# Kernel tuning notes

Measured on AMD Instinct MI355X. Metric: run time of the kernel, lower is better.

## Reference

```python
import jax, jax.numpy as jnp
import numpy as np
import math

# neuralef_loss_cfg constants
T = 10.0
K_FEAT = 32          # num_nearestn_feature
K_PIX = ((10, 2.0), (10, 0.1))  # (num_nearestn_pixel{1,2}, distance_weight)
PIX_W = 0.05         # pixelwise_weight
ALPHA = 1.0


def setup_inputs() -> dict:
    key = jax.random.key(0)
    k1, k2, k3 = jax.random.split(key, 3)
    highlevel_feature = jax.random.normal(k1, (8, 1024, 768), dtype=jnp.float32)
    Psi = jax.random.normal(k2, (8, 1024, 64), dtype=jnp.float32)
    im = jax.random.normal(k3, (8, 3, 32, 32), dtype=jnp.float32)
    return {"highlevel_feature": highlevel_feature, "Psi": Psi, "im": im}


def _build_gram(highlevel_feature, im):
    """Feature kNN graph + pixel kNN graphs -> degree-normalized gram matrix."""
    bs, n, d = highlevel_feature.shape
    M = bs * n
    # --- feature affinity: cosine sim, mutual-ish kNN sparsification ---
    X = highlevel_feature.reshape(M, d)
    X = X / jnp.linalg.norm(X, axis=-1, keepdims=True)
    A = X @ X.T                                   # [M, M]
    A = A.at[jnp.diag_indices(M)].set(-jnp.inf)
    A = jnp.maximum(A, 0.0)                       # clamp(min=0); diag -inf -> 0
    vals, idx = jax.lax.top_k(A, K_FEAT)          # [M, K]
    res = jnp.zeros_like(A).at[jnp.arange(M)[:, None], idx].set(vals)
    A = (res + res.T) * 0.5

    # --- pixel affinity: RGB + weighted xy coordinates, euclidean kNN ---
    im = (im + 1.0) / 2.0
    h, w = im.shape[2], im.shape[3]
    hw = h * w
    x_ = jnp.tile(jnp.linspace(0.0, 1.0, w), (h,))          # [hw]
    y_ = jnp.repeat(jnp.linspace(0.0, 1.0, h), w)           # [hw]
    imf = im.reshape(bs, 3, hw).transpose(0, 2, 1)          # [bs, hw, 3]
    row = jnp.arange(hw)
    A_p = jnp.zeros((bs, hw, hw), dtype=bool)
    for k, dw in K_PIX:
        if k == 0:
            continue
        coords = jnp.broadcast_to(jnp.stack([x_ * dw, y_ * dw], -1), (bs, hw, 2))
        im2 = jnp.concatenate([imf, coords], axis=-1)       # [bs, hw, 5]
        sq = jnp.sum(im2 * im2, axis=-1)                    # [bs, hw]
        d2 = sq[:, :, None] + sq[:, None, :] - 2.0 * jnp.einsum('bnd,bmd->bnm', im2, im2)
        euc = -jnp.sqrt(jnp.maximum(d2, 0.0))               # -cdist
        euc = euc.at[:, row, row].set(-jnp.inf)
        _, pidx = jax.lax.top_k(euc, k)                     # [bs, hw, k]
        r = jnp.zeros((bs, hw, hw), dtype=bool).at[
            jnp.arange(bs)[:, None, None], row[None, :, None], pidx].set(True)
        A_p = A_p | r | r.transpose(0, 2, 1)

    A2 = jax.scipy.linalg.block_diag(*[A_p[i].astype(jnp.float32) for i in range(bs)])

    D = jax.lax.rsqrt(A.sum(-1))
    gram = A * D[None, :] * D[:, None]
    D2 = jax.lax.rsqrt(A2.sum(-1))
    gram2 = A2 * D2[None, :] * D2[:, None]
    return gram + gram2 * PIX_W                             # [M, M]


def reference(highlevel_feature, Psi, im):
    Psi = Psi.reshape(-1, Psi.shape[-1]) * math.sqrt(T)     # [M, kdim]
    gram = _build_gram(highlevel_feature, im)
    gP = gram @ Psi                                         # [M, kdim]
    R = Psi.T @ gP
    R_hat = jax.lax.stop_gradient(Psi).T @ gP               # no_sg = False
    kdim = Psi.shape[1]
    loss = -jnp.trace(R) / kdim
    reg = jnp.sum(jnp.triu(R_hat ** 2, 1)) / kdim
    return (loss, reg * ALPHA)
```

## Files before the change

kernel.cpp:

```cpp
#include <hip/hip_runtime.h>
#include <hip/hip_bf16.h>
#include <math.h>

constexpr int MT  = 8192;
constexpr int DF  = 768;
constexpr int KD  = 64;
constexpr int HWP = 1024;
constexpr int KF  = 32;
constexpr int KP  = 10;
constexpr int RPB = 512;
constexpr int CANDQ = 512;
constexpr int NTILE = 2080;
#define SQT 3.16227766016837933f
#define PIXW 0.05f
#define THR_BITS 0x2C7Bu

typedef __bf16 bf16x8 __attribute__((ext_vector_type(8)));
typedef __bf16 bf16x4 __attribute__((ext_vector_type(4)));
typedef float  f32x4  __attribute__((ext_vector_type(4)));
typedef unsigned u32x4 __attribute__((ext_vector_type(4)));
typedef unsigned short u16x8 __attribute__((ext_vector_type(8)));
typedef _Float16 f16;

__device__ inline void tile_map(int bid, int& ti, int& tj) {
  const int xcd = bid & 7;
  const int s = bid >> 3;
  const int p = s / 65, r = s % 65;
  const int c1 = xcd * 4 + p;
  if (r <= c1) { ti = r; tj = c1; }
  else         { ti = r - c1 - 1; tj = 63 - c1; }
}

__global__ __launch_bounds__(256) void prep_input_kernel(const float* __restrict__ X,
                                                         __bf16* __restrict__ Xb,
                                                         const float* __restrict__ im,
                                                         unsigned* __restrict__ pmask,
                                                         float* __restrict__ frow) {
  __shared__ float fr[HWP], fg[HWP], fb[HWP];
  __shared__ float red[256];
  const int tid = threadIdx.x;
  if (blockIdx.x < MT) {
    const int row = blockIdx.x;
    if (tid == 0) frow[row] = 0.f;
    const float4* xr4 = (const float4*)(X + (size_t)row * DF);
    float4 v = make_float4(0.f, 0.f, 0.f, 0.f);
    float s = 0.f;
    if (tid < 192) {
      v = xr4[tid];
      s = v.x * v.x + v.y * v.y + v.z * v.z + v.w * v.w;
    }
    red[tid] = s; __syncthreads();
    for (int o = 128; o > 0; o >>= 1) { if (tid < o) red[tid] += red[tid + o]; __syncthreads(); }
    const float rn = rsqrtf(red[0]);
    if (tid < 192) {
      bf16x4 o;
      o[0] = (__bf16)(v.x * rn); o[1] = (__bf16)(v.y * rn);
      o[2] = (__bf16)(v.z * rn); o[3] = (__bf16)(v.w * rn);
      *(bf16x4*)(Xb + (size_t)row * DF + tid * 4) = o;
    }
    return;
  }
  const int bx = blockIdx.x - MT;
  const int lane = tid & 63, wv = tid >> 6;
  const int b = bx >> 8;
  const int p = ((bx & 255) << 2) + wv;
  const float* imb = im + (size_t)b * 3 * HWP;
  for (int q = tid; q < HWP; q += 256) {
    fr[q] = imb[q]; fg[q] = imb[HWP + q]; fb[q] = imb[2 * HWP + q];
  }
  __syncthreads();
  const float pr = fr[p], pg = fg[p], pb = fb[p];
  const float px = (float)(p & 31) * (1.f / 31.f), py = (float)(p >> 5) * (1.f / 31.f);
  float d0[16], d1[16];
  #pragma unroll
  for (int i = 0; i < 16; ++i) {
    const int q = lane + (i << 6);
    float dr = (fr[q] - pr) * 0.5f, dg = (fg[q] - pg) * 0.5f, db = (fb[q] - pb) * 0.5f;
    float drgb = dr * dr + dg * dg + db * db;
    float dx = (float)(q & 31) * (1.f / 31.f) - px;
    float dy = (float)(q >> 5) * (1.f / 31.f) - py;
    float cd = dx * dx + dy * dy;
    d0[i] = (q == p) ? 1e30f : drgb + 4.00f * cd;
    d1[i] = (q == p) ? 1e30f : drgb + 0.01f * cd;
  }
  const int mrow = (b << 10) + p;
  auto doPass = [&](float (&dd)[16]) {
    for (int it = 0; it < KP; ++it) {
      float bm = 1e30f; int bq = 0;
      #pragma unroll
      for (int i = 0; i < 16; ++i) {
        const int q = lane + (i << 6);
        if (dd[i] < bm) { bm = dd[i]; bq = q; }
      }
      #pragma unroll
      for (int o = 32; o > 0; o >>= 1) {
        float ov = __shfl_down(bm, o);
        int   oq = __shfl_down(bq, o);
        if (ov < bm) { bm = ov; bq = oq; }
      }
      bq = __shfl(bq, 0);
      if (lane == 0) {
        atomicOr(&pmask[(size_t)mrow * 32 + (bq >> 5)], 1u << (bq & 31));
        atomicOr(&pmask[((size_t)((b << 10) + bq)) * 32 + (p >> 5)], 1u << (p & 31));
      }
      #pragma unroll
      for (int i = 0; i < 16; ++i)
        if (lane + (i << 6) == bq) dd[i] = 1e30f;
    }
  };
  doPass(d0);
  doPass(d1);
}

union SMem {
  struct { __bf16 A[128 * 64]; __bf16 B[128 * 64]; } st;
  f16 T[128 * 128];
};

__global__ __launch_bounds__(256) void gemm_kernel(const __bf16* __restrict__ Xb,
                                                   f16* __restrict__ S) {
  __shared__ SMem sm;
  const int tid = threadIdx.x;
  const int lane = tid & 63;
  const int wv = tid >> 6;
  const int wm = (wv & 1) * 64, wn = (wv >> 1) * 64;
  const int l15 = lane & 15, lq = lane >> 4;
  const int lr8 = lane >> 3, lc8 = lane & 7;
  const int rsw = l15 & 7;

  int ti, tj;
  tile_map(blockIdx.x, ti, tj);
  const int m0 = ti * 128;
  const int n0 = tj * 128;

  f32x4 acc[4][4];
  #pragma unroll
  for (int i = 0; i < 4; ++i)
    #pragma unroll
    for (int j = 0; j < 4; ++j)
      #pragma unroll
      for (int q = 0; q < 4; ++q) acc[i][j][q] = 0.f;

  for (int kt = 0; kt < 12; ++kt) {
    const int col0 = kt * 64;
    const __bf16* Ag = Xb + (size_t)m0 * DF + col0;
    const __bf16* Bg = Xb + (size_t)n0 * DF + col0;
    #pragma unroll
    for (int i = 0; i < 4; ++i) {
      const int r0 = (wv * 4 + i) * 8;
      const int csw = (lc8 ^ lr8) * 8;
      __builtin_amdgcn_global_load_lds(
          (const __attribute__((address_space(1))) void*)(Ag + (size_t)(r0 + lr8) * DF + csw),
          (__attribute__((address_space(3))) void*)(&sm.st.A[r0 * 64]), 16, 0, 0);
      __builtin_amdgcn_global_load_lds(
          (const __attribute__((address_space(1))) void*)(Bg + (size_t)(r0 + lr8) * DF + csw),
          (__attribute__((address_space(3))) void*)(&sm.st.B[r0 * 64]), 16, 0, 0);
    }
    __syncthreads();
    #pragma unroll
    for (int kk = 0; kk < 64; kk += 32) {
      bf16x8 af[4], bg[4];
      #pragma unroll
      for (int i = 0; i < 4; ++i)
        af[i] = *(const bf16x8*)(&sm.st.A[(wm + i * 16 + l15) * 64 + ((((kk >> 3) + lq) ^ rsw) * 8)]);
      #pragma unroll
      for (int j = 0; j < 4; ++j)
        bg[j] = *(const bf16x8*)(&sm.st.B[(wn + j * 16 + l15) * 64 + ((((kk >> 3) + lq) ^ rsw) * 8)]);
      #pragma unroll
      for (int i = 0; i < 4; ++i)
        #pragma unroll
        for (int j = 0; j < 4; ++j)
          acc[i][j] = __builtin_amdgcn_mfma_f32_16x16x32_bf16(af[i], bg[j], acc[i][j], 0, 0, 0);
    }
    __syncthreads();
  }
  #pragma unroll
  for (int i = 0; i < 4; ++i)
    #pragma unroll
    for (int j = 0; j < 4; ++j)
      #pragma unroll
      for (int q = 0; q < 4; ++q) {
        const int tr = wm + i * 16 + lq * 4 + q;
        const int tc = wn + j * 16 + l15;
        sm.T[tr * 128 + ((((tc >> 3) ^ (tr & 7)) << 3) | (tc & 7))] = (f16)acc[i][j][q];
      }
  __syncthreads();
  for (int e = tid; e < 128 * 16; e += 256) {
    const int r = e >> 4, ch = e & 15;
    const u32x4 v = *(const u32x4*)&sm.T[r * 128 + ((ch ^ (r & 7)) << 3)];
    __builtin_nontemporal_store(v, (u32x4*)&S[(size_t)(m0 + r) * MT + n0 + ch * 8]);
  }
  if (m0 != n0) {
    __syncthreads();
    #pragma unroll
    for (int i = 0; i < 4; ++i)
      #pragma unroll
      for (int j = 0; j < 4; ++j)
        #pragma unroll
        for (int q = 0; q < 4; ++q) {
          const int tr = wm + i * 16 + lq * 4 + q;
          const int tc = wn + j * 16 + l15;
          sm.T[tc * 128 + ((((tr >> 3) ^ (tc & 7)) << 3) | (tr & 7))] = (f16)acc[i][j][q];
        }
    __syncthreads();
    for (int e = tid; e < 128 * 16; e += 256) {
      const int r = e >> 4, ch = e & 15;
      const u32x4 v = *(const u32x4*)&sm.T[r * 128 + ((ch ^ (r & 7)) << 3)];
      __builtin_nontemporal_store(v, (u32x4*)&S[(size_t)(n0 + r) * MT + m0 + ch * 8]);
    }
  }
}

__global__ __launch_bounds__(256) void select_kernel(const f16* __restrict__ S,
                                                     int* __restrict__ fidx,
                                                     float* __restrict__ fval,
                                                     float* __restrict__ frow) {
  __shared__ alignas(16) unsigned cp[CANDQ];
  __shared__ int wcnt[4];
  __shared__ float srow;
  const int tid = threadIdx.x;
  const int row = blockIdx.x;
  const int wv = tid >> 6, lane = tid & 63;
  if (tid == 0) srow = 0.f;
  const unsigned long long ltmask = (1ULL << lane) - 1ULL;
  const u16x8* srow8 = (const u16x8*)(S + (size_t)row * MT);
  u16x8 pk[4];
  #pragma unroll
  for (int i = 0; i < 4; ++i) pk[i] = srow8[i * 256 + tid];
  unsigned tot = 0;
  #pragma unroll
  for (int i = 0; i < 4; ++i)
    #pragma unroll
    for (int j = 0; j < 8; ++j) {
      const unsigned u = pk[i][j];
      const int c = i * 2048 + tid * 8 + j;
      const unsigned long long bal = __ballot(u >= THR_BITS && u < 0x8000u && c != row);
      tot += (unsigned)__popcll(bal);
    }
  if (lane == 0) wcnt[wv] = (int)tot;
  __syncthreads();
  int base = 0, ntot = 0;
  #pragma unroll
  for (int w = 0; w < 4; ++w) {
    if (w < wv) base += wcnt[w];
    ntot += wcnt[w];
  }
  const int n = min(ntot, CANDQ);
  const int npad = (n + 7) & ~7;
  int run = base;
  #pragma unroll
  for (int i = 0; i < 4; ++i)
    #pragma unroll
    for (int j = 0; j < 8; ++j) {
      const unsigned u = pk[i][j];
      const int c = i * 2048 + tid * 8 + j;
      const bool pred = (u >= THR_BITS && u < 0x8000u && c != row);
      const unsigned long long bal = __ballot(pred);
      if (pred) {
        const int pos = run + (int)__popcll(bal & ltmask);
        if (pos < CANDQ) cp[pos] = (u << 16) | (unsigned)(8191 - c);
      }
      run += (int)__popcll(bal);
    }
  for (int e = n + tid; e < npad; e += 256) cp[e] = 0u;
  __syncthreads();
  for (int e = tid; e < n; e += 256) {
    const unsigned me = cp[e];
    int rank = 0;
    for (int j = 0; j < npad; j += 8) {
      const u32x4 a = *(const u32x4*)&cp[j];
      const u32x4 b = *(const u32x4*)&cp[j + 4];
      rank += (a[0] > me) + (a[1] > me) + (a[2] > me) + (a[3] > me) +
              (b[0] > me) + (b[1] > me) + (b[2] > me) + (b[3] > me);
    }
    if (rank < KF) {
      union { unsigned short us; f16 h; } cvu; cvu.us = (unsigned short)(me >> 16);
      const float vv = (float)cvu.h;
      const int idx = 8191 - (int)(me & 0x1fffu);
      fval[(size_t)row * KF + rank] = vv;
      fidx[(size_t)row * KF + rank] = idx;
      atomicAdd(&frow[idx], 0.5f * vv);
      atomicAdd(&srow, 0.5f * vv);
    }
  }
  for (int rk = n + tid; rk < KF; rk += 256) {
    fval[(size_t)row * KF + rk] = 0.f;
    fidx[(size_t)row * KF + rk] = row;
  }
  __syncthreads();
  if (tid == 0) atomicAdd(&frow[row], srow);
}

__global__ void scales_kernel(const float* __restrict__ frow,
                              const unsigned* __restrict__ pmask,
                              float* __restrict__ sf, float* __restrict__ sp,
                              float* __restrict__ Rm) {
  int m = blockIdx.x * blockDim.x + threadIdx.x;
  if (m < KD * KD) Rm[m] = 0.f;
  if (m >= MT) return;
  const u32x4* pm = (const u32x4*)(pmask + (size_t)m * 32);
  int deg = 0;
  #pragma unroll
  for (int w = 0; w < 8; ++w) {
    const u32x4 bits = pm[w];
    deg += __popc(bits[0]) + __popc(bits[1]) + __popc(bits[2]) + __popc(bits[3]);
  }
  const float fr = frow[m];
  sf[m] = (fr > 0.f) ? rsqrtf(fr) * SQT : 0.f;
  sp[m] = (deg > 0) ? rsqrtf((float)deg) * SQT : 0.f;
}

__global__ __launch_bounds__(256) void gather_kernel(const int* __restrict__ fidx,
                                                     const float* __restrict__ fval,
                                                     const float* __restrict__ sf,
                                                     const float* __restrict__ sp,
                                                     const unsigned* __restrict__ pmask,
                                                     const float* __restrict__ Psi,
                                                     float* __restrict__ Wf,
                                                     float* __restrict__ W2) {
  __shared__ int list[4][64];
  __shared__ int cnts[4];
  const int w = threadIdx.x >> 6;
  const int t = threadIdx.x & 63;
  const int m = blockIdx.x * 4 + w;
  const int b = m >> 10;
  if (t == 0) cnts[w] = 0;
  __syncthreads();
  if (t < 32) {
    unsigned bits = pmask[(size_t)m * 32 + t];
    while (bits) {
      int bit = __ffs(bits) - 1;
      bits &= bits - 1;
      int pos = atomicAdd(&cnts[w], 1);
      if (pos < 64) list[w][pos] = t * 32 + bit;
    }
  }
  __syncthreads();
  float accf = 0.f;
  for (int k = 0; k < KF; ++k) {
    const float v = fval[m * KF + k];
    const int   c = fidx[m * KF + k];
    accf += 0.5f * v * sf[c] * Psi[(size_t)c * KD + t];
  }
  Wf[(size_t)m * KD + t] = accf;
  const int n = min(cnts[w], 64);
  float accp = 0.f;
  for (int e = 0; e < n; ++e) {
    const int g = b * HWP + list[w][e];
    accp += sp[g] * Psi[(size_t)g * KD + t];
  }
  W2[(size_t)m * KD + t] = accp;
}

__global__ __launch_bounds__(256) void rmat_part_kernel(const float* __restrict__ Psi,
                                                        const float* __restrict__ sf,
                                                        const float* __restrict__ sp,
                                                        const float* __restrict__ Wf,
                                                        const float* __restrict__ W2,
                                                        float* __restrict__ Pf,
                                                        float* __restrict__ Pp) {
  __shared__ float sPsi[8][KD], sWf[8][KD], sW2[8][KD];
  __shared__ float ssf[8], ssp[8];
  const int tid = threadIdx.x;
  const int c = tid & 63, g = tid >> 6;
  float accf[16], accp[16];
  #pragma unroll
  for (int i = 0; i < 16; ++i) { accf[i] = 0.f; accp[i] = 0.f; }
  const int rowBeg = blockIdx.x * (MT / RPB);
  for (int r0 = rowBeg; r0 < rowBeg + MT / RPB; r0 += 8) {
    #pragma unroll
    for (int e = tid; e < 8 * KD; e += 256) {
      const int r = e >> 6, cc = e & 63;
      const size_t gi = (size_t)(r0 + r) * KD + cc;
      sPsi[r][cc] = Psi[gi];
      sWf[r][cc]  = Wf[gi];
      sW2[r][cc]  = W2[gi];
    }
    if (tid < 8) { ssf[tid] = sf[r0 + tid]; ssp[tid] = sp[r0 + tid]; }
    __syncthreads();
    #pragma unroll
    for (int r = 0; r < 8; ++r) {
      const float wf = sWf[r][c], w2 = sW2[r][c];
      const float fsc = ssf[r], psc = ssp[r];
      const f32x4* p4 = (const f32x4*)&sPsi[r][g * 16];
      #pragma unroll
      for (int q = 0; q < 4; ++q) {
        const f32x4 pp = p4[q];
        #pragma unroll
        for (int k = 0; k < 4; ++k) {
          accf[q * 4 + k] += fsc * pp[k] * wf;
          accp[q * 4 + k] += psc * pp[k] * w2;
        }
      }
    }
    __syncthreads();
  }
  float* pf = Pf + (size_t)blockIdx.x * KD * KD;
  float* pp = Pp + (size_t)blockIdx.x * KD * KD;
  #pragma unroll
  for (int i = 0; i < 16; ++i) {
    const int a = g * 16 + i;
    pf[a * KD + c] = accf[i];
    pp[a * KD + c] = accp[i];
  }
}

__global__ __launch_bounds__(256) void rmat_reduce_kernel(const float* __restrict__ Pf,
                                                          const float* __restrict__ Pp,
                                                          float* __restrict__ Rm) {
  const int e = (blockIdx.x & 15) * 256 + threadIdx.x;
  const int grp = blockIdx.x >> 4;
  const int a = e >> 6, c = e & 63;
  const int eT = c * KD + a;
  float f = 0.f, ft = 0.f, p = 0.f;
  #pragma unroll 8
  for (int b = grp * 128; b < grp * 128 + 128; ++b) {
    f  += Pf[(size_t)b * KD * KD + e];
    ft += Pf[(size_t)b * KD * KD + eT];
    p  += Pp[(size_t)b * KD * KD + e];
  }
  atomicAdd(&Rm[e], f + ft + PIXW * p);
}

__global__ __launch_bounds__(256) void final_kernel(const float* __restrict__ Rm,
                                                    float* __restrict__ out) {
  __shared__ float redt[256], redr[256];
  const int tid = threadIdx.x;
  float tr = 0.f, rg = 0.f;
  for (int e = tid; e < KD * KD; e += 256) {
    int a = e >> 6, c = e & 63;
    float v = Rm[e];
    if (a == c) tr += v;
    else if (c > a) rg += v * v;
  }
  redt[tid] = tr; redr[tid] = rg;
  __syncthreads();
  for (int o = 128; o > 0; o >>= 1) {
    if (tid < o) { redt[tid] += redt[tid + o]; redr[tid] += redr[tid + o]; }
    __syncthreads();
  }
  if (tid == 0) {
    out[0] = -redt[0] / (float)KD;
    out[1] = redr[0] / (float)KD;
  }
}

extern "C" void kernel_launch(void* const* d_in, const int* in_sizes, int n_in,
                              void* d_out, int out_size, void* d_ws, size_t ws_size,
                              hipStream_t stream) {
  const float* hl  = (const float*)d_in[0];
  const float* Psi = (const float*)d_in[1];
  const float* im  = (const float*)d_in[2];
  float* out = (float*)d_out;

  char* ws = (char*)d_ws;
  size_t off = 0;
  auto alloc = [&](size_t bytes) -> void* {
    void* p = ws + off;
    off = (off + bytes + 255) & ~(size_t)255;
    return p;
  };
  f16*      S     = (f16*)alloc((size_t)MT * MT * 2);
  __bf16*   Xb    = (__bf16*)alloc((size_t)MT * DF * 2);
  int*      fidx  = (int*)alloc((size_t)MT * KF * 4);
  float*    fval  = (float*)alloc((size_t)MT * KF * 4);
  float*    frow  = (float*)alloc((size_t)MT * 4);
  float*    sf    = (float*)alloc((size_t)MT * 4);
  float*    sp    = (float*)alloc((size_t)MT * 4);
  unsigned* pmask = (unsigned*)alloc((size_t)MT * 32 * 4);
  float*    Wf    = (float*)alloc((size_t)MT * KD * 4);
  float*    W2    = (float*)alloc((size_t)MT * KD * 4);
  float*    Pf    = (float*)alloc((size_t)RPB * KD * KD * 4);
  float*    Pp    = (float*)alloc((size_t)RPB * KD * KD * 4);
  float*    Rm    = (float*)alloc((size_t)KD * KD * 4);

  hipMemsetAsync(pmask, 0, (size_t)MT * 32 * 4, stream);

  prep_input_kernel<<<MT + MT / 4, 256, 0, stream>>>(hl, Xb, im, pmask, frow);
  gemm_kernel<<<NTILE, 256, 0, stream>>>(Xb, S);
  select_kernel<<<MT, 256, 0, stream>>>(S, fidx, fval, frow);
  scales_kernel<<<MT / 256, 256, 0, stream>>>(frow, pmask, sf, sp, Rm);
  gather_kernel<<<MT / 4, 256, 0, stream>>>(fidx, fval, sf, sp, pmask, Psi, Wf, W2);
  rmat_part_kernel<<<RPB, 256, 0, stream>>>(Psi, sf, sp, Wf, W2, Pf, Pp);
  rmat_reduce_kernel<<<64, 256, 0, stream>>>(Pf, Pp, Rm);
  final_kernel<<<1, 256, 0, stream>>>(Rm, out);
}
```

Before: 337.1 us.

## Replace ballot compaction with per-thread masks, shrink gather blocks, halve rmat partials

The select kernel now builds a per-thread candidate bitmask once and uses a wavefront shuffle prefix sum for compaction, replacing 32 ballot/popcount steps done in each of two passes. The gather kernel launches one 64-thread block per row instead of four rows per 256-thread block, which removes cross-wave barrier coupling. The rmat partial count drops from 512 to 256 blocks, with the reduce loop adjusted to match, so less partial data is written and read back. The trade-off is less parallelism in rmat_part and more, smaller blocks in gather.

```diff
diff --git a/kernel.cpp b/kernel.cpp
--- a/kernel.cpp
+++ b/kernel.cpp
@@ -8,7 +8,7 @@
 constexpr int HWP = 1024;
 constexpr int KF  = 32;
 constexpr int KP  = 10;
-constexpr int RPB = 512;
+constexpr int RPB = 256;
 constexpr int CANDQ = 512;
 constexpr int NTILE = 2080;
 #define SQT 3.16227766016837933f
@@ -222,22 +222,27 @@
   const int row = blockIdx.x;
   const int wv = tid >> 6, lane = tid & 63;
   if (tid == 0) srow = 0.f;
-  const unsigned long long ltmask = (1ULL << lane) - 1ULL;
   const u16x8* srow8 = (const u16x8*)(S + (size_t)row * MT);
   u16x8 pk[4];
   #pragma unroll
   for (int i = 0; i < 4; ++i) pk[i] = srow8[i * 256 + tid];
-  unsigned tot = 0;
+  unsigned msk = 0;
   #pragma unroll
   for (int i = 0; i < 4; ++i)
     #pragma unroll
     for (int j = 0; j < 8; ++j) {
       const unsigned u = pk[i][j];
       const int c = i * 2048 + tid * 8 + j;
-      const unsigned long long bal = __ballot(u >= THR_BITS && u < 0x8000u && c != row);
-      tot += (unsigned)__popcll(bal);
-    }
-  if (lane == 0) wcnt[wv] = (int)tot;
+      if (u >= THR_BITS && u < 0x8000u && c != row) msk |= 1u << (i * 8 + j);
+    }
+  const int cnt = __popc(msk);
+  int x = cnt;
+  #pragma unroll
+  for (int o = 1; o < 64; o <<= 1) {
+    const int y = __shfl_up(x, o);
+    if (lane >= o) x += y;
+  }
+  if (lane == 63) wcnt[wv] = x;
   __syncthreads();
   int base = 0, ntot = 0;
   #pragma unroll
@@ -247,21 +252,19 @@
   }
   const int n = min(ntot, CANDQ);
   const int npad = (n + 7) & ~7;
-  int run = base;
+  int pos = base + x - cnt;
   #pragma unroll
   for (int i = 0; i < 4; ++i)
     #pragma unroll
-    for (int j = 0; j < 8; ++j) {
-      const unsigned u = pk[i][j];
-      const int c = i * 2048 + tid * 8 + j;
-      const bool pred = (u >= THR_BITS && u < 0x8000u && c != row);
-      const unsigned long long bal = __ballot(pred);
-      if (pred) {
-        const int pos = run + (int)__popcll(bal & ltmask);
-        if (pos < CANDQ) cp[pos] = (u << 16) | (unsigned)(8191 - c);
-      }
-      run += (int)__popcll(bal);
-    }
+    for (int j = 0; j < 8; ++j)
+      if (msk & (1u << (i * 8 + j))) {
+        if (pos < CANDQ) {
+          const unsigned u = pk[i][j];
+          const int c = i * 2048 + tid * 8 + j;
+          cp[pos] = (u << 16) | (unsigned)(8191 - c);
+        }
+        ++pos;
+      }
   for (int e = n + tid; e < npad; e += 256) cp[e] = 0u;
   __syncthreads();
   for (int e = tid; e < n; e += 256) {
@@ -310,29 +313,28 @@
   sp[m] = (deg > 0) ? rsqrtf((float)deg) * SQT : 0.f;
 }
 
-__global__ __launch_bounds__(256) void gather_kernel(const int* __restrict__ fidx,
-                                                     const float* __restrict__ fval,
-                                                     const float* __restrict__ sf,
-                                                     const float* __restrict__ sp,
-                                                     const unsigned* __restrict__ pmask,
-                                                     const float* __restrict__ Psi,
-                                                     float* __restrict__ Wf,
-                                                     float* __restrict__ W2) {
-  __shared__ int list[4][64];
-  __shared__ int cnts[4];
-  const int w = threadIdx.x >> 6;
-  const int t = threadIdx.x & 63;
-  const int m = blockIdx.x * 4 + w;
+__global__ __launch_bounds__(64) void gather_kernel(const int* __restrict__ fidx,
+                                                    const float* __restrict__ fval,
+                                                    const float* __restrict__ sf,
+                                                    const float* __restrict__ sp,
+                                                    const unsigned* __restrict__ pmask,
+                                                    const float* __restrict__ Psi,
+                                                    float* __restrict__ Wf,
+                                                    float* __restrict__ W2) {
+  __shared__ int list[64];
+  __shared__ int cnt;
+  const int m = blockIdx.x;
+  const int t = threadIdx.x;
   const int b = m >> 10;
-  if (t == 0) cnts[w] = 0;
+  if (t == 0) cnt = 0;
   __syncthreads();
   if (t < 32) {
     unsigned bits = pmask[(size_t)m * 32 + t];
     while (bits) {
       int bit = __ffs(bits) - 1;
       bits &= bits - 1;
-      int pos = atomicAdd(&cnts[w], 1);
-      if (pos < 64) list[w][pos] = t * 32 + bit;
+      int pos = atomicAdd(&cnt, 1);
+      if (pos < 64) list[pos] = t * 32 + bit;
     }
   }
   __syncthreads();
@@ -343,10 +345,10 @@
     accf += 0.5f * v * sf[c] * Psi[(size_t)c * KD + t];
   }
   Wf[(size_t)m * KD + t] = accf;
-  const int n = min(cnts[w], 64);
+  const int n = min(cnt, 64);
   float accp = 0.f;
   for (int e = 0; e < n; ++e) {
-    const int g = b * HWP + list[w][e];
+    const int g = b * HWP + list[e];
     accp += sp[g] * Psi[(size_t)g * KD + t];
   }
   W2[(size_t)m * KD + t] = accp;
@@ -414,7 +416,7 @@
   const int eT = c * KD + a;
   float f = 0.f, ft = 0.f, p = 0.f;
   #pragma unroll 8
-  for (int b = grp * 128; b < grp * 128 + 128; ++b) {
+  for (int b = grp * 64; b < grp * 64 + 64; ++b) {
     f  += Pf[(size_t)b * KD * KD + e];
     ft += Pf[(size_t)b * KD * KD + eT];
     p  += Pp[(size_t)b * KD * KD + e];
@@ -480,7 +482,7 @@
   gemm_kernel<<<NTILE, 256, 0, stream>>>(Xb, S);
   select_kernel<<<MT, 256, 0, stream>>>(S, fidx, fval, frow);
   scales_kernel<<<MT / 256, 256, 0, stream>>>(frow, pmask, sf, sp, Rm);
-  gather_kernel<<<MT / 4, 256, 0, stream>>>(fidx, fval, sf, sp, pmask, Psi, Wf, W2);
+  gather_kernel<<<MT, 64, 0, stream>>>(fidx, fval, sf, sp, pmask, Psi, Wf, W2);
   rmat_part_kernel<<<RPB, 256, 0, stream>>>(Psi, sf, sp, Wf, W2, Pf, Pp);
   rmat_reduce_kernel<<<64, 256, 0, stream>>>(Pf, Pp, Rm);
   final_kernel<<<1, 256, 0, stream>>>(Rm, out);
```

Result: faster. 310.0 us (-8.1%).
